# Kernel optimization log

Measured on AMD Instinct MI355X. Metric: run time of the kernel, lower is better.

Reference implementation:

```python
import jax, jax.numpy as jnp
import numpy as np

B, T = 16, 8192
V, CE, CR, CS = 256, 256, 128, 256
L = 12
GC = CR // 2  # gate channels
K = 2


def causal_conv(x, w, b, dilation):
    # x: [B,C_in,T], w: [C_out,C_in,K] -> [B,C_out,T], left-padded (causal)
    pad = (w.shape[-1] - 1) * dilation
    y = jax.lax.conv_general_dilated(
        x, w, window_strides=(1,), padding=[(pad, 0)],
        rhs_dilation=(dilation,), dimension_numbers=('NCH', 'OIH', 'NCH'))
    return y + b[None, :, None]


def pw(x, w, b):
    # 1x1 conv: x [B,Ci,T], w [Co,Ci] -> [B,Co,T]
    return jnp.einsum('oi,bit->bot', w, x) + b[None, :, None]


def setup_inputs() -> dict:
    key = jax.random.key(0)
    ks = jax.random.split(key, 12)
    s = 0.05
    return {
        'tokens': jax.random.randint(ks[0], (B, T), 0, V),
        'emb': jax.random.normal(ks[1], (V, CE), jnp.float32) * s,
        'w_init': jax.random.normal(ks[2], (CR, CE, K), jnp.float32) * s,
        'b_init': jnp.zeros((CR,), jnp.float32),
        'w_dil': jax.random.normal(ks[3], (L, CR, CR, K), jnp.float32) * s,
        'b_dil': jnp.zeros((L, CR), jnp.float32),
        'w_res': jax.random.normal(ks[4], (L, CR, GC), jnp.float32) * s,
        'b_res': jnp.zeros((L, CR), jnp.float32),
        'w_skip': jax.random.normal(ks[5], (L, CS, GC), jnp.float32) * s,
        'b_skip': jnp.zeros((L, CS), jnp.float32),
        'w_out1': jax.random.normal(ks[6], (CS, CS), jnp.float32) * s,
        'b_out1': jnp.zeros((CS,), jnp.float32),
        'w_out2': jax.random.normal(ks[7], (V, CS), jnp.float32) * s,
        'b_out2': jnp.zeros((V,), jnp.float32),
    }


def reference(tokens, emb, w_init, b_init, w_dil, b_dil, w_res, b_res,
              w_skip, b_skip, w_out1, b_out1, w_out2, b_out2):
    # embedding -> [B,CE,T]
    h = emb[tokens].transpose(0, 2, 1)
    # initial causal conv: k=2, dilation=1
    x = causal_conv(h, w_init, b_init, 1)
    skip_sum = jnp.zeros((B, CS, T), x.dtype)
    # NOTE: due to swapped positional args in the torch source, every block's
    # dilated conv has kernel_size=2 and dilation=2.
    for i in range(L):
        xc = causal_conv(x, w_dil[i], b_dil[i], 2)
        g = jnp.tanh(xc[:, :GC, :]) * jax.nn.sigmoid(xc[:, GC:, :])
        skip_sum = skip_sum + pw(g, w_skip[i], b_skip[i])
        x = pw(g, w_res[i], b_res[i]) + x
    s = skip_sum / L  # stack(...).sum(0)/len == mean
    s = pw(jax.nn.relu(s), w_out1, b_out1)
    return pw(jax.nn.relu(s), w_out2, b_out2)  # [B,V,T]
```

## Files before the change

kernel.cpp:

```cpp
#include <hip/hip_runtime.h>


typedef __attribute__((ext_vector_type(8))) short short8;
typedef __attribute__((ext_vector_type(4))) short short4v;
typedef __attribute__((ext_vector_type(4))) float f32x4;

#define T_TOK 8192
#define TT    128
#define HALO  32
#define XSTE  136
#define GSTE  72
#define SSTE  264
#define X_OFF 0
#define G_OFF 43520
#define S_OFF 0
#define LDS_BYTES 67584

#define FI  0
#define FD  65536
#define FS  458752
#define FR  655360
#define FO1 753664
#define FO2 819200
#define FRAG_TOTAL 884736
#define BSK_BYTE_OFF  (FRAG_TOTAL * 2)
#define EMBF_BYTE_OFF (BSK_BYTE_OFF + 1024)
#define PREP_TOTAL (FRAG_TOTAL + 256 + 65536)

#define MFMA(a, b, c) __builtin_amdgcn_mfma_f32_16x16x32_bf16(a, b, c, 0, 0, 0)

__device__ __forceinline__ unsigned short f2b(float f) {
  unsigned int x = __builtin_bit_cast(unsigned int, f);
  return (unsigned short)((x + 0x7fffu + ((x >> 16) & 1u)) >> 16);
}

__global__ void __launch_bounds__(256) prep_kernel(
    const float* __restrict__ emb,
    const float* __restrict__ w_init,
    const float* __restrict__ w_dil,
    const float* __restrict__ w_skip,
    const float* __restrict__ w_res,
    const float* __restrict__ w_out1,
    const float* __restrict__ w_out2,
    const float* __restrict__ b_skip,
    unsigned short* __restrict__ frags,
    float* __restrict__ bsk,
    unsigned short* __restrict__ embf)
{
  int flat = blockIdx.x * 256 + threadIdx.x;
  if (flat < FRAG_TOTAL) {
    float val;
    if (flat < FD) {
      int rel = flat;
      int j = rel & 7, lane = (rel >> 3) & 63, outer = rel >> 9;
      int kc = outer & 7, mt = (outer >> 3) & 7, tap = outer >> 6;
      int m = mt * 16 + (lane & 15);
      int k = kc * 32 + (lane >> 4) * 8 + j;
      val = w_init[(m * 256 + k) * 2 + tap];
    } else if (flat < FS) {
      int rel = flat - FD;
      int j = rel & 7, lane = (rel >> 3) & 63, outer = rel >> 9;
      int kc = outer & 3, mt = (outer >> 2) & 7, tap = (outer >> 5) & 1, l = outer >> 6;
      int m = mt * 16 + (lane & 15);
      int k = kc * 32 + (lane >> 4) * 8 + j;
      val = w_dil[((l * 128 + m) * 128 + k) * 2 + tap];
    } else if (flat < FR) {
      int rel = flat - FS;
      int j = rel & 7, lane = (rel >> 3) & 63, outer = rel >> 9;
      int kc = outer & 1, mt = (outer >> 1) & 15, l = outer >> 5;
      int m = mt * 16 + (lane & 15);
      int k = kc * 32 + (lane >> 4) * 8 + j;
      val = w_skip[(l * 256 + m) * 64 + k] * (1.0f / 12.0f);
    } else if (flat < FO1) {
      int rel = flat - FR;
      int j = rel & 7, lane = (rel >> 3) & 63, outer = rel >> 9;
      int kc = outer & 1, mt = (outer >> 1) & 7, l = outer >> 4;
      int m = mt * 16 + (lane & 15);
      int k = kc * 32 + (lane >> 4) * 8 + j;
      val = w_res[(l * 128 + m) * 64 + k];
    } else if (flat < FO2) {
      int rel = flat - FO1;
      int j = rel & 7, lane = (rel >> 3) & 63, outer = rel >> 9;
      int kc = outer & 7, mt = outer >> 3;
      int m = mt * 16 + (lane & 15);
      int k = kc * 32 + (lane >> 4) * 8 + j;
      val = w_out1[m * 256 + k];
    } else {
      int rel = flat - FO2;
      int j = rel & 7, lane = (rel >> 3) & 63, outer = rel >> 9;
      int kc = outer & 7, mt = outer >> 3;
      int m = mt * 16 + (lane & 15);
      int k = kc * 32 + (lane >> 4) * 8 + j;
      val = w_out2[m * 256 + k];
    }
    frags[flat] = f2b(val);
  } else if (flat < FRAG_TOTAL + 256) {
    int ch = flat - FRAG_TOTAL;
    float s = 0.f;
    for (int l = 0; l < 12; l++) s += b_skip[l * 256 + ch];
    bsk[ch] = s * (1.0f / 12.0f);
  } else if (flat < PREP_TOTAL) {
    int i = flat - FRAG_TOTAL - 256;
    embf[i] = f2b(emb[i]);
  }
}

extern "C" __global__ void __launch_bounds__(512, 4) wavenet_main(
    const int* __restrict__ tokens,
    const unsigned short* __restrict__ embf,
    const unsigned short* __restrict__ frags,
    const float* __restrict__ bsk,
    const float* __restrict__ b_init,
    const float* __restrict__ b_dil,
    const float* __restrict__ b_res,
    const float* __restrict__ b_out1,
    const float* __restrict__ b_out2,
    float* __restrict__ out)
{
  extern __shared__ char lds[];
  unsigned short* xb = (unsigned short*)(lds + X_OFF);
  unsigned short* gb = (unsigned short*)(lds + G_OFF);
  unsigned short* sb = (unsigned short*)(lds + S_OFF);

  const int tid = threadIdx.x;
  const int lane = tid & 63;
  const int w = tid >> 6;
  const int l16 = lane & 15;
  const int q = lane >> 4;
  const int wm = w & 3;
  const int wn = w >> 2;
  const int bb = blockIdx.x >> 6;
  const int chunk = blockIdx.x & 63;
  const int tb = chunk * TT - HALO;

  int ncol[5];
#pragma unroll
  for (int jn = 0; jn < 5; jn++) ncol[jn] = (wn * 5 + jn) * 16 + l16;

  const short8 zero8 = {0, 0, 0, 0, 0, 0, 0, 0};
  f32x4 acc[2][5];
  f32x4 sk[2][8];

  int tk[5][2];
#pragma unroll
  for (int jn = 0; jn < 5; jn++) {
#pragma unroll
    for (int s = 0; s < 2; s++) {
      int shift = s ? 0 : 1;
      int tsrc = tb + ncol[jn] - shift;
      tk[jn][s] = (tsrc >= 0) ? tokens[bb * T_TOK + tsrc] : -1;
    }
  }
#pragma unroll
  for (int i = 0; i < 2; i++) {
    f32x4 bv;
#pragma unroll
    for (int r = 0; r < 4; r++) bv[r] = b_init[(wm + 4 * i) * 16 + q * 4 + r];
#pragma unroll
    for (int jn = 0; jn < 5; jn++) acc[i][jn] = bv;
  }
#pragma unroll
  for (int s = 0; s < 2; s++) {
#pragma unroll
    for (int kc = 0; kc < 8; kc++) {
      short8 a0 = *(const short8*)(frags + FI + (((s * 8 + wm    ) * 8 + kc) * 64 + lane) * 8);
      short8 a1 = *(const short8*)(frags + FI + (((s * 8 + wm + 4) * 8 + kc) * 64 + lane) * 8);
#pragma unroll
      for (int jn = 0; jn < 5; jn++) {
        int t = tk[jn][s];
        int ts = t < 0 ? 0 : t;
        short8 bv = *(const short8*)(embf + ts * 256 + kc * 32 + q * 8);
        if (t < 0) bv = zero8;
        acc[0][jn] = MFMA(a0, bv, acc[0][jn]);
        acc[1][jn] = MFMA(a1, bv, acc[1][jn]);
      }
    }
  }
#pragma unroll
  for (int i = 0; i < 2; i++) {
#pragma unroll
    for (int jn = 0; jn < 5; jn++) {
      short4v pk;
#pragma unroll
      for (int r = 0; r < 4; r++) pk[r] = (short)f2b(acc[i][jn][r]);
      if (tb + ncol[jn] < 0) { pk[0] = 0; pk[1] = 0; pk[2] = 0; pk[3] = 0; }
      *(short4v*)(xb + ncol[jn] * XSTE + (wm + 4 * i) * 16 + q * 4) = pk;
    }
  }
#pragma unroll
  for (int i = 0; i < 2; i++) {
    f32x4 bv;
#pragma unroll
    for (int r = 0; r < 4; r++) bv[r] = bsk[(2 * w + i) * 16 + q * 4 + r];
#pragma unroll
    for (int jt = 0; jt < 8; jt++) sk[i][jt] = bv;
  }
  __syncthreads();

  for (int layer = 0; layer < 12; layer++) {
#pragma unroll
    for (int i = 0; i < 2; i++) {
      f32x4 bv;
#pragma unroll
      for (int r = 0; r < 4; r++) bv[r] = b_dil[layer * 128 + (wm + 4 * i) * 16 + q * 4 + r];
#pragma unroll
      for (int jn = 0; jn < 5; jn++) acc[i][jn] = bv;
    }
#pragma unroll
    for (int s = 0; s < 2; s++) {
      const int shift = s ? 0 : 2;
#pragma unroll
      for (int kc = 0; kc < 4; kc++) {
        short8 a0 = *(const short8*)(frags + FD + ((((layer * 2 + s) * 8 + wm    ) * 4 + kc) * 64 + lane) * 8);
        short8 a1 = *(const short8*)(frags + FD + ((((layer * 2 + s) * 8 + wm + 4) * 4 + kc) * 64 + lane) * 8);
#pragma unroll
        for (int jn = 0; jn < 5; jn++) {
          int c = ncol[jn] - shift; if (c < 0) c = 0;
          short8 bv = *(const short8*)(xb + c * XSTE + kc * 32 + q * 8);
          acc[0][jn] = MFMA(a0, bv, acc[0][jn]);
          acc[1][jn] = MFMA(a1, bv, acc[1][jn]);
        }
      }
    }
#pragma unroll
    for (int jn = 0; jn < 5; jn++) {
      short4v pk;
#pragma unroll
      for (int r = 0; r < 4; r++) {
        float xt = acc[0][jn][r];
        float xs = acc[1][jn][r];
        float th = 1.f - 2.f / (__expf(2.f * xt) + 1.f);
        float sg = 1.f / (1.f + __expf(-xs));
        pk[r] = (short)f2b(th * sg);
      }
      if (tb + ncol[jn] < 0) { pk[0] = 0; pk[1] = 0; pk[2] = 0; pk[3] = 0; }
      *(short4v*)(gb + ncol[jn] * GSTE + wm * 16 + q * 4) = pk;
    }
    __syncthreads();
#pragma unroll
    for (int kc = 0; kc < 2; kc++) {
      short8 a0 = *(const short8*)(frags + FS + (((layer * 16 + 2 * w    ) * 2 + kc) * 64 + lane) * 8);
      short8 a1 = *(const short8*)(frags + FS + (((layer * 16 + 2 * w + 1) * 2 + kc) * 64 + lane) * 8);
#pragma unroll
      for (int jt = 0; jt < 8; jt++) {
        short8 bv = *(const short8*)(gb + (HALO + jt * 16 + l16) * GSTE + kc * 32 + q * 8);
        sk[0][jt] = MFMA(a0, bv, sk[0][jt]);
        sk[1][jt] = MFMA(a1, bv, sk[1][jt]);
      }
    }
#pragma unroll
    for (int i = 0; i < 2; i++) {
      f32x4 bv;
#pragma unroll
      for (int r = 0; r < 4; r++) bv[r] = b_res[layer * 128 + (wm + 4 * i) * 16 + q * 4 + r];
#pragma unroll
      for (int jn = 0; jn < 5; jn++) acc[i][jn] = bv;
    }
#pragma unroll
    for (int kc = 0; kc < 2; kc++) {
      short8 a0 = *(const short8*)(frags + FR + (((layer * 8 + wm    ) * 2 + kc) * 64 + lane) * 8);
      short8 a1 = *(const short8*)(frags + FR + (((layer * 8 + wm + 4) * 2 + kc) * 64 + lane) * 8);
#pragma unroll
      for (int jn = 0; jn < 5; jn++) {
        short8 bv = *(const short8*)(gb + ncol[jn] * GSTE + kc * 32 + q * 8);
        acc[0][jn] = MFMA(a0, bv, acc[0][jn]);
        acc[1][jn] = MFMA(a1, bv, acc[1][jn]);
      }
    }
#pragma unroll
    for (int i = 0; i < 2; i++) {
#pragma unroll
      for (int jn = 0; jn < 5; jn++) {
        unsigned short* p = xb + ncol[jn] * XSTE + (wm + 4 * i) * 16 + q * 4;
        short4v old = *(short4v*)p;
        short4v pk;
#pragma unroll
        for (int r = 0; r < 4; r++) {
          float xo = __builtin_bit_cast(float, (unsigned int)(unsigned short)old[r] << 16);
          pk[r] = (short)f2b(acc[i][jn][r] + xo);
        }
        if (tb + ncol[jn] < 0) { pk[0] = 0; pk[1] = 0; pk[2] = 0; pk[3] = 0; }
        *(short4v*)p = pk;
      }
    }
    __syncthreads();
  }

#pragma unroll
  for (int i = 0; i < 2; i++) {
#pragma unroll
    for (int jt = 0; jt < 8; jt++) {
      short4v pk;
#pragma unroll
      for (int r = 0; r < 4; r++) pk[r] = (short)f2b(fmaxf(sk[i][jt][r], 0.f));
      *(short4v*)(sb + (jt * 16 + l16) * SSTE + (2 * w + i) * 16 + q * 4) = pk;
    }
  }
  __syncthreads();
#pragma unroll
  for (int i = 0; i < 2; i++) {
    f32x4 bv;
#pragma unroll
    for (int r = 0; r < 4; r++) bv[r] = b_out1[(2 * w + i) * 16 + q * 4 + r];
#pragma unroll
    for (int jt = 0; jt < 8; jt++) sk[i][jt] = bv;
  }
#pragma unroll
  for (int kc = 0; kc < 8; kc++) {
    short8 a0 = *(const short8*)(frags + FO1 + (((2 * w    ) * 8 + kc) * 64 + lane) * 8);
    short8 a1 = *(const short8*)(frags + FO1 + (((2 * w + 1) * 8 + kc) * 64 + lane) * 8);
#pragma unroll
    for (int jt = 0; jt < 8; jt++) {
      short8 bv = *(const short8*)(sb + (jt * 16 + l16) * SSTE + kc * 32 + q * 8);
      sk[0][jt] = MFMA(a0, bv, sk[0][jt]);
      sk[1][jt] = MFMA(a1, bv, sk[1][jt]);
    }
  }
  short4v t1p[2][8];
#pragma unroll
  for (int i = 0; i < 2; i++) {
#pragma unroll
    for (int jt = 0; jt < 8; jt++) {
#pragma unroll
      for (int r = 0; r < 4; r++) t1p[i][jt][r] = (short)f2b(fmaxf(sk[i][jt][r], 0.f));
    }
  }
  __syncthreads();
#pragma unroll
  for (int i = 0; i < 2; i++) {
#pragma unroll
    for (int jt = 0; jt < 8; jt++)
      *(short4v*)(sb + (jt * 16 + l16) * SSTE + (2 * w + i) * 16 + q * 4) = t1p[i][jt];
  }
  __syncthreads();
#pragma unroll
  for (int i = 0; i < 2; i++) {
    f32x4 bv;
#pragma unroll
    for (int r = 0; r < 4; r++) bv[r] = b_out2[(2 * w + i) * 16 + q * 4 + r];
#pragma unroll
    for (int jt = 0; jt < 8; jt++) sk[i][jt] = bv;
  }
#pragma unroll
  for (int kc = 0; kc < 8; kc++) {
    short8 a0 = *(const short8*)(frags + FO2 + (((2 * w    ) * 8 + kc) * 64 + lane) * 8);
    short8 a1 = *(const short8*)(frags + FO2 + (((2 * w + 1) * 8 + kc) * 64 + lane) * 8);
#pragma unroll
    for (int jt = 0; jt < 8; jt++) {
      short8 bv = *(const short8*)(sb + (jt * 16 + l16) * SSTE + kc * 32 + q * 8);
      sk[0][jt] = MFMA(a0, bv, sk[0][jt]);
      sk[1][jt] = MFMA(a1, bv, sk[1][jt]);
    }
  }
  const int t0 = chunk * TT;
#pragma unroll
  for (int i = 0; i < 2; i++) {
#pragma unroll
    for (int jt = 0; jt < 8; jt++) {
#pragma unroll
      for (int r = 0; r < 4; r++) {
        int v = (2 * w + i) * 16 + q * 4 + r;
        int t = t0 + jt * 16 + l16;
        out[((size_t)(bb * 256 + v) << 13) + t] = sk[i][jt][r];
      }
    }
  }
}

extern "C" void kernel_launch(void* const* d_in, const int* in_sizes, int n_in,
                              void* d_out, int out_size, void* d_ws, size_t ws_size,
                              hipStream_t stream) {
  (void)in_sizes; (void)n_in; (void)out_size; (void)ws_size;
  const int*   tokens = (const int*)d_in[0];
  const float* emb    = (const float*)d_in[1];
  const float* w_init = (const float*)d_in[2];
  const float* b_init = (const float*)d_in[3];
  const float* w_dil  = (const float*)d_in[4];
  const float* b_dil  = (const float*)d_in[5];
  const float* w_res  = (const float*)d_in[6];
  const float* b_res  = (const float*)d_in[7];
  const float* w_skip = (const float*)d_in[8];
  const float* b_skip = (const float*)d_in[9];
  const float* w_out1 = (const float*)d_in[10];
  const float* b_out1 = (const float*)d_in[11];
  const float* w_out2 = (const float*)d_in[12];
  const float* b_out2 = (const float*)d_in[13];

  unsigned short* frags = (unsigned short*)d_ws;
  float* bsk = (float*)((char*)d_ws + BSK_BYTE_OFF);
  unsigned short* embf = (unsigned short*)((char*)d_ws + EMBF_BYTE_OFF);

  prep_kernel<<<dim3(PREP_TOTAL / 256), dim3(256), 0, stream>>>(
      emb, w_init, w_dil, w_skip, w_res, w_out1, w_out2, b_skip,
      frags, bsk, embf);

  (void)hipFuncSetAttribute((const void*)wavenet_main,
                            hipFuncAttributeMaxDynamicSharedMemorySize, LDS_BYTES);

  wavenet_main<<<dim3(1024), dim3(512), LDS_BYTES, stream>>>(
      tokens, embf, frags, bsk, b_init, b_dil, b_res, b_out1, b_out2,
      (float*)d_out);
}
```

Measured before the change: 678.4 us.

## Split column tiles into groups, use hardware bf16 pack and cheaper gate math

The per-warp column tiles are processed in two groups of 3 and 2 via templated helpers, so fewer accumulators are live at once and register pressure drops under the 4-blocks-per-CU launch bound. Software round-to-nearest bf16 conversion is replaced by the v_cvt_pk_bf16_f32 instruction. The tanh*sigmoid gate is rewritten to use a single reciprocal with a clamp, and bias loads are vectorised. Splitting means the weight fragments are reloaded once per group, and the fused gate formula may differ slightly in rounding.

New measurement: 639.3 us. -5.8%, faster.

```diff
diff --git a/kernel.cpp b/kernel.cpp
--- a/kernel.cpp
+++ b/kernel.cpp
@@ -2,8 +2,8 @@
 
 
 typedef __attribute__((ext_vector_type(8))) short short8;
-typedef __attribute__((ext_vector_type(4))) short short4v;
 typedef __attribute__((ext_vector_type(4))) float f32x4;
+typedef __attribute__((ext_vector_type(2))) unsigned int uint2v;
 
 #define T_TOK 8192
 #define TT    128
@@ -32,6 +32,12 @@
 __device__ __forceinline__ unsigned short f2b(float f) {
   unsigned int x = __builtin_bit_cast(unsigned int, f);
   return (unsigned short)((x + 0x7fffu + ((x >> 16) & 1u)) >> 16);
+}
+
+__device__ __forceinline__ unsigned int cvt_pk_bf16(float lo, float hi) {
+  unsigned int r;
+  asm("v_cvt_pk_bf16_f32 %0, %1, %2" : "=v"(r) : "v"(lo), "v"(hi));
+  return r;
 }
 
 __global__ void __launch_bounds__(256) prep_kernel(
@@ -105,6 +111,154 @@
   }
 }
 
+
+template<int G0, int GN>
+__device__ __forceinline__ void phaseA_grp(
+    const int* __restrict__ tokens, const unsigned short* __restrict__ embf,
+    const unsigned short* __restrict__ frags, const float* __restrict__ b_init,
+    unsigned short* __restrict__ xb,
+    int bb, int tb, int colbase, int wm, int lane, int q)
+{
+  const short8 zero8 = {0, 0, 0, 0, 0, 0, 0, 0};
+  int tk[GN][2];
+#pragma unroll
+  for (int jn = 0; jn < GN; jn++) {
+    int col = colbase + (G0 + jn) * 16;
+#pragma unroll
+    for (int s = 0; s < 2; s++) {
+      int shift = s ? 0 : 1;
+      int tsrc = tb + col - shift;
+      tk[jn][s] = (tsrc >= 0) ? tokens[bb * T_TOK + tsrc] : -1;
+    }
+  }
+  f32x4 acc[2][GN];
+#pragma unroll
+  for (int i = 0; i < 2; i++) {
+    f32x4 bv = *(const f32x4*)(b_init + (wm + 4 * i) * 16 + q * 4);
+#pragma unroll
+    for (int jn = 0; jn < GN; jn++) acc[i][jn] = bv;
+  }
+#pragma unroll
+  for (int s = 0; s < 2; s++) {
+#pragma unroll
+    for (int kc = 0; kc < 8; kc++) {
+      short8 a0 = *(const short8*)(frags + FI + (((s * 8 + wm    ) * 8 + kc) * 64 + lane) * 8);
+      short8 a1 = *(const short8*)(frags + FI + (((s * 8 + wm + 4) * 8 + kc) * 64 + lane) * 8);
+#pragma unroll
+      for (int jn = 0; jn < GN; jn++) {
+        int t = tk[jn][s];
+        int ts = t < 0 ? 0 : t;
+        short8 bv = *(const short8*)(embf + ts * 256 + kc * 32 + q * 8);
+        if (t < 0) bv = zero8;
+        acc[0][jn] = MFMA(a0, bv, acc[0][jn]);
+        acc[1][jn] = MFMA(a1, bv, acc[1][jn]);
+      }
+    }
+  }
+#pragma unroll
+  for (int i = 0; i < 2; i++) {
+#pragma unroll
+    for (int jn = 0; jn < GN; jn++) {
+      int col = colbase + (G0 + jn) * 16;
+      unsigned int u0 = cvt_pk_bf16(acc[i][jn][0], acc[i][jn][1]);
+      unsigned int u1 = cvt_pk_bf16(acc[i][jn][2], acc[i][jn][3]);
+      if (tb + col < 0) { u0 = 0; u1 = 0; }
+      *(uint2v*)(xb + col * XSTE + (wm + 4 * i) * 16 + q * 4) = (uint2v){u0, u1};
+    }
+  }
+}
+
+template<int G0, int GN>
+__device__ __forceinline__ void dil_gate_grp(
+    const unsigned short* __restrict__ frags, const float* __restrict__ b_dil,
+    const unsigned short* __restrict__ xb, unsigned short* __restrict__ gb,
+    int layer, int tb, int colbase, int wm, int lane, int q)
+{
+  f32x4 acc[2][GN];
+#pragma unroll
+  for (int i = 0; i < 2; i++) {
+    f32x4 bv = *(const f32x4*)(b_dil + layer * 128 + (wm + 4 * i) * 16 + q * 4);
+#pragma unroll
+    for (int jn = 0; jn < GN; jn++) acc[i][jn] = bv;
+  }
+#pragma unroll
+  for (int s = 0; s < 2; s++) {
+    const int shift = s ? 0 : 2;
+#pragma unroll
+    for (int kc = 0; kc < 4; kc++) {
+      short8 a0 = *(const short8*)(frags + FD + ((((layer * 2 + s) * 8 + wm    ) * 4 + kc) * 64 + lane) * 8);
+      short8 a1 = *(const short8*)(frags + FD + ((((layer * 2 + s) * 8 + wm + 4) * 4 + kc) * 64 + lane) * 8);
+#pragma unroll
+      for (int jn = 0; jn < GN; jn++) {
+        int c = colbase + (G0 + jn) * 16 - shift; if (c < 0) c = 0;
+        short8 bv = *(const short8*)(xb + c * XSTE + kc * 32 + q * 8);
+        acc[0][jn] = MFMA(a0, bv, acc[0][jn]);
+        acc[1][jn] = MFMA(a1, bv, acc[1][jn]);
+      }
+    }
+  }
+#pragma unroll
+  for (int jn = 0; jn < GN; jn++) {
+    int col = colbase + (G0 + jn) * 16;
+    float g[4];
+#pragma unroll
+    for (int r = 0; r < 4; r++) {
+      float xt = fminf(acc[0][jn][r], 40.f);
+      float A = __expf(2.f * xt);
+      float Bs = __expf(-acc[1][jn][r]);
+      g[r] = (A - 1.f) * __builtin_amdgcn_rcpf((A + 1.f) * (1.f + Bs));
+    }
+    unsigned int u0 = cvt_pk_bf16(g[0], g[1]);
+    unsigned int u1 = cvt_pk_bf16(g[2], g[3]);
+    if (tb + col < 0) { u0 = 0; u1 = 0; }
+    *(uint2v*)(gb + col * GSTE + wm * 16 + q * 4) = (uint2v){u0, u1};
+  }
+}
+
+template<int G0, int GN>
+__device__ __forceinline__ void res_upd_grp(
+    const unsigned short* __restrict__ frags, const float* __restrict__ b_res,
+    unsigned short* __restrict__ xb, const unsigned short* __restrict__ gb,
+    int layer, int tb, int colbase, int wm, int lane, int q)
+{
+  f32x4 acc[2][GN];
+#pragma unroll
+  for (int i = 0; i < 2; i++) {
+    f32x4 bv = *(const f32x4*)(b_res + layer * 128 + (wm + 4 * i) * 16 + q * 4);
+#pragma unroll
+    for (int jn = 0; jn < GN; jn++) acc[i][jn] = bv;
+  }
+#pragma unroll
+  for (int kc = 0; kc < 2; kc++) {
+    short8 a0 = *(const short8*)(frags + FR + (((layer * 8 + wm    ) * 2 + kc) * 64 + lane) * 8);
+    short8 a1 = *(const short8*)(frags + FR + (((layer * 8 + wm + 4) * 2 + kc) * 64 + lane) * 8);
+#pragma unroll
+    for (int jn = 0; jn < GN; jn++) {
+      int col = colbase + (G0 + jn) * 16;
+      short8 bv = *(const short8*)(gb + col * GSTE + kc * 32 + q * 8);
+      acc[0][jn] = MFMA(a0, bv, acc[0][jn]);
+      acc[1][jn] = MFMA(a1, bv, acc[1][jn]);
+    }
+  }
+#pragma unroll
+  for (int i = 0; i < 2; i++) {
+#pragma unroll
+    for (int jn = 0; jn < GN; jn++) {
+      int col = colbase + (G0 + jn) * 16;
+      unsigned short* p = xb + col * XSTE + (wm + 4 * i) * 16 + q * 4;
+      uint2v old = *(const uint2v*)p;
+      float x0 = __builtin_bit_cast(float, old[0] << 16);
+      float x1 = __builtin_bit_cast(float, old[0] & 0xffff0000u);
+      float x2 = __builtin_bit_cast(float, old[1] << 16);
+      float x3 = __builtin_bit_cast(float, old[1] & 0xffff0000u);
+      unsigned int u0 = cvt_pk_bf16(acc[i][jn][0] + x0, acc[i][jn][1] + x1);
+      unsigned int u1 = cvt_pk_bf16(acc[i][jn][2] + x2, acc[i][jn][3] + x3);
+      if (tb + col < 0) { u0 = 0; u1 = 0; }
+      *(uint2v*)p = (uint2v){u0, u1};
+    }
+  }
+}
+
 extern "C" __global__ void __launch_bounds__(512, 4) wavenet_main(
     const int* __restrict__ tokens,
     const unsigned short* __restrict__ embf,
@@ -132,110 +286,24 @@
   const int bb = blockIdx.x >> 6;
   const int chunk = blockIdx.x & 63;
   const int tb = chunk * TT - HALO;
-
-  int ncol[5];
-#pragma unroll
-  for (int jn = 0; jn < 5; jn++) ncol[jn] = (wn * 5 + jn) * 16 + l16;
-
-  const short8 zero8 = {0, 0, 0, 0, 0, 0, 0, 0};
-  f32x4 acc[2][5];
+  const int colbase = wn * 80 + l16;
+
   f32x4 sk[2][8];
 
-  int tk[5][2];
-#pragma unroll
-  for (int jn = 0; jn < 5; jn++) {
-#pragma unroll
-    for (int s = 0; s < 2; s++) {
-      int shift = s ? 0 : 1;
-      int tsrc = tb + ncol[jn] - shift;
-      tk[jn][s] = (tsrc >= 0) ? tokens[bb * T_TOK + tsrc] : -1;
-    }
-  }
-#pragma unroll
-  for (int i = 0; i < 2; i++) {
-    f32x4 bv;
-#pragma unroll
-    for (int r = 0; r < 4; r++) bv[r] = b_init[(wm + 4 * i) * 16 + q * 4 + r];
-#pragma unroll
-    for (int jn = 0; jn < 5; jn++) acc[i][jn] = bv;
-  }
-#pragma unroll
-  for (int s = 0; s < 2; s++) {
-#pragma unroll
-    for (int kc = 0; kc < 8; kc++) {
-      short8 a0 = *(const short8*)(frags + FI + (((s * 8 + wm    ) * 8 + kc) * 64 + lane) * 8);
-      short8 a1 = *(const short8*)(frags + FI + (((s * 8 + wm + 4) * 8 + kc) * 64 + lane) * 8);
-#pragma unroll
-      for (int jn = 0; jn < 5; jn++) {
-        int t = tk[jn][s];
-        int ts = t < 0 ? 0 : t;
-        short8 bv = *(const short8*)(embf + ts * 256 + kc * 32 + q * 8);
-        if (t < 0) bv = zero8;
-        acc[0][jn] = MFMA(a0, bv, acc[0][jn]);
-        acc[1][jn] = MFMA(a1, bv, acc[1][jn]);
-      }
-    }
-  }
-#pragma unroll
-  for (int i = 0; i < 2; i++) {
-#pragma unroll
-    for (int jn = 0; jn < 5; jn++) {
-      short4v pk;
-#pragma unroll
-      for (int r = 0; r < 4; r++) pk[r] = (short)f2b(acc[i][jn][r]);
-      if (tb + ncol[jn] < 0) { pk[0] = 0; pk[1] = 0; pk[2] = 0; pk[3] = 0; }
-      *(short4v*)(xb + ncol[jn] * XSTE + (wm + 4 * i) * 16 + q * 4) = pk;
-    }
-  }
-#pragma unroll
-  for (int i = 0; i < 2; i++) {
-    f32x4 bv;
-#pragma unroll
-    for (int r = 0; r < 4; r++) bv[r] = bsk[(2 * w + i) * 16 + q * 4 + r];
+  phaseA_grp<0, 3>(tokens, embf, frags, b_init, xb, bb, tb, colbase, wm, lane, q);
+  phaseA_grp<3, 2>(tokens, embf, frags, b_init, xb, bb, tb, colbase, wm, lane, q);
+
+#pragma unroll
+  for (int i = 0; i < 2; i++) {
+    f32x4 bv = *(const f32x4*)(bsk + (2 * w + i) * 16 + q * 4);
 #pragma unroll
     for (int jt = 0; jt < 8; jt++) sk[i][jt] = bv;
   }
   __syncthreads();
 
   for (int layer = 0; layer < 12; layer++) {
-#pragma unroll
-    for (int i = 0; i < 2; i++) {
-      f32x4 bv;
-#pragma unroll
-      for (int r = 0; r < 4; r++) bv[r] = b_dil[layer * 128 + (wm + 4 * i) * 16 + q * 4 + r];
-#pragma unroll
-      for (int jn = 0; jn < 5; jn++) acc[i][jn] = bv;
-    }
-#pragma unroll
-    for (int s = 0; s < 2; s++) {
-      const int shift = s ? 0 : 2;
-#pragma unroll
-      for (int kc = 0; kc < 4; kc++) {
-        short8 a0 = *(const short8*)(frags + FD + ((((layer * 2 + s) * 8 + wm    ) * 4 + kc) * 64 + lane) * 8);
-        short8 a1 = *(const short8*)(frags + FD + ((((layer * 2 + s) * 8 + wm + 4) * 4 + kc) * 64 + lane) * 8);
-#pragma unroll
-        for (int jn = 0; jn < 5; jn++) {
-          int c = ncol[jn] - shift; if (c < 0) c = 0;
-          short8 bv = *(const short8*)(xb + c * XSTE + kc * 32 + q * 8);
-          acc[0][jn] = MFMA(a0, bv, acc[0][jn]);
-          acc[1][jn] = MFMA(a1, bv, acc[1][jn]);
-        }
-      }
-    }
-#pragma unroll
-    for (int jn = 0; jn < 5; jn++) {
-      short4v pk;
-#pragma unroll
-      for (int r = 0; r < 4; r++) {
-        float xt = acc[0][jn][r];
-        float xs = acc[1][jn][r];
-        float th = 1.f - 2.f / (__expf(2.f * xt) + 1.f);
-        float sg = 1.f / (1.f + __expf(-xs));
-        pk[r] = (short)f2b(th * sg);
-      }
-      if (tb + ncol[jn] < 0) { pk[0] = 0; pk[1] = 0; pk[2] = 0; pk[3] = 0; }
-      *(short4v*)(gb + ncol[jn] * GSTE + wm * 16 + q * 4) = pk;
-    }
+    dil_gate_grp<0, 3>(frags, b_dil, xb, gb, layer, tb, colbase, wm, lane, q);
+    dil_gate_grp<3, 2>(frags, b_dil, xb, gb, layer, tb, colbase, wm, lane, q);
     __syncthreads();
 #pragma unroll
     for (int kc = 0; kc < 2; kc++) {
@@ -248,41 +316,8 @@
         sk[1][jt] = MFMA(a1, bv, sk[1][jt]);
       }
     }
-#pragma unroll
-    for (int i = 0; i < 2; i++) {
-      f32x4 bv;
-#pragma unroll
-      for (int r = 0; r < 4; r++) bv[r] = b_res[layer * 128 + (wm + 4 * i) * 16 + q * 4 + r];
-#pragma unroll
-      for (int jn = 0; jn < 5; jn++) acc[i][jn] = bv;
-    }
-#pragma unroll
-    for (int kc = 0; kc < 2; kc++) {
-      short8 a0 = *(const short8*)(frags + FR + (((layer * 8 + wm    ) * 2 + kc) * 64 + lane) * 8);
-      short8 a1 = *(const short8*)(frags + FR + (((layer * 8 + wm + 4) * 2 + kc) * 64 + lane) * 8);
-#pragma unroll
-      for (int jn = 0; jn < 5; jn++) {
-        short8 bv = *(const short8*)(gb + ncol[jn] * GSTE + kc * 32 + q * 8);
-        acc[0][jn] = MFMA(a0, bv, acc[0][jn]);
-        acc[1][jn] = MFMA(a1, bv, acc[1][jn]);
-      }
-    }
-#pragma unroll
-    for (int i = 0; i < 2; i++) {
-#pragma unroll
-      for (int jn = 0; jn < 5; jn++) {
-        unsigned short* p = xb + ncol[jn] * XSTE + (wm + 4 * i) * 16 + q * 4;
-        short4v old = *(short4v*)p;
-        short4v pk;
-#pragma unroll
-        for (int r = 0; r < 4; r++) {
-          float xo = __builtin_bit_cast(float, (unsigned int)(unsigned short)old[r] << 16);
-          pk[r] = (short)f2b(acc[i][jn][r] + xo);
-        }
-        if (tb + ncol[jn] < 0) { pk[0] = 0; pk[1] = 0; pk[2] = 0; pk[3] = 0; }
-        *(short4v*)p = pk;
-      }
-    }
+    res_upd_grp<0, 3>(frags, b_res, xb, gb, layer, tb, colbase, wm, lane, q);
+    res_upd_grp<3, 2>(frags, b_res, xb, gb, layer, tb, colbase, wm, lane, q);
     __syncthreads();
   }
 
@@ -290,18 +325,15 @@
   for (int i = 0; i < 2; i++) {
 #pragma unroll
     for (int jt = 0; jt < 8; jt++) {
-      short4v pk;
-#pragma unroll
-      for (int r = 0; r < 4; r++) pk[r] = (short)f2b(fmaxf(sk[i][jt][r], 0.f));
-      *(short4v*)(sb + (jt * 16 + l16) * SSTE + (2 * w + i) * 16 + q * 4) = pk;
+      unsigned int u0 = cvt_pk_bf16(fmaxf(sk[i][jt][0], 0.f), fmaxf(sk[i][jt][1], 0.f));
+      unsigned int u1 = cvt_pk_bf16(fmaxf(sk[i][jt][2], 0.f), fmaxf(sk[i][jt][3], 0.f));
+      *(uint2v*)(sb + (jt * 16 + l16) * SSTE + (2 * w + i) * 16 + q * 4) = (uint2v){u0, u1};
     }
   }
   __syncthreads();
 #pragma unroll
   for (int i = 0; i < 2; i++) {
-    f32x4 bv;
-#pragma unroll
-    for (int r = 0; r < 4; r++) bv[r] = b_out1[(2 * w + i) * 16 + q * 4 + r];
+    f32x4 bv = *(const f32x4*)(b_out1 + (2 * w + i) * 16 + q * 4);
 #pragma unroll
     for (int jt = 0; jt < 8; jt++) sk[i][jt] = bv;
   }
@@ -316,13 +348,13 @@
       sk[1][jt] = MFMA(a1, bv, sk[1][jt]);
     }
   }
-  short4v t1p[2][8];
+  unsigned int t1p[2][8][2];
 #pragma unroll
   for (int i = 0; i < 2; i++) {
 #pragma unroll
     for (int jt = 0; jt < 8; jt++) {
-#pragma unroll
-      for (int r = 0; r < 4; r++) t1p[i][jt][r] = (short)f2b(fmaxf(sk[i][jt][r], 0.f));
+      t1p[i][jt][0] = cvt_pk_bf16(fmaxf(sk[i][jt][0], 0.f), fmaxf(sk[i][jt][1], 0.f));
+      t1p[i][jt][1] = cvt_pk_bf16(fmaxf(sk[i][jt][2], 0.f), fmaxf(sk[i][jt][3], 0.f));
     }
   }
   __syncthreads();
@@ -330,14 +362,13 @@
   for (int i = 0; i < 2; i++) {
 #pragma unroll
     for (int jt = 0; jt < 8; jt++)
-      *(short4v*)(sb + (jt * 16 + l16) * SSTE + (2 * w + i) * 16 + q * 4) = t1p[i][jt];
+      *(uint2v*)(sb + (jt * 16 + l16) * SSTE + (2 * w + i) * 16 + q * 4) =
+          (uint2v){t1p[i][jt][0], t1p[i][jt][1]};
   }
   __syncthreads();
 #pragma unroll
   for (int i = 0; i < 2; i++) {
-    f32x4 bv;
-#pragma unroll
-    for (int r = 0; r < 4; r++) bv[r] = b_out2[(2 * w + i) * 16 + q * 4 + r];
+    f32x4 bv = *(const f32x4*)(b_out2 + (2 * w + i) * 16 + q * 4);
 #pragma unroll
     for (int jt = 0; jt < 8; jt++) sk[i][jt] = bv;
   }
```
